# Optimization experiments

Measured on AMD Instinct MI355X. Metric: run time of the kernel, lower is better.

The kernel has to match this reference:

```python
import jax, jax.numpy as jnp
import numpy as np

SCALING = 32.0 / 16.0  # alpha / rank

def setup_inputs() -> dict:
    key = jax.random.key(0)
    ks = jax.random.split(key, 6)
    B, S, D_IN, D_OUT, R, N_ADAPT = 32, 1024, 1024, 4096, 16, 8
    hidden_states = jax.random.normal(ks[0], (B, S, D_IN), dtype=jnp.float32)
    adapter_ids = jax.random.randint(ks[1], (B,), 0, N_ADAPT, dtype=jnp.int32)
    W = jax.random.normal(ks[2], (D_IN, D_OUT), dtype=jnp.float32) * 0.02
    bias = jax.random.normal(ks[3], (D_OUT,), dtype=jnp.float32) * 0.02
    lora_a = jax.random.normal(ks[4], (N_ADAPT, D_IN, R), dtype=jnp.float32) * (1.0 / np.sqrt(D_IN))
    lora_b = jax.random.normal(ks[5], (N_ADAPT, R, D_OUT), dtype=jnp.float32) * 0.02
    return {"hidden_states": hidden_states, "adapter_ids": adapter_ids,
            "W": W, "bias": bias, "lora_a": lora_a, "lora_b": lora_b}

def reference(hidden_states, adapter_ids, W, bias, lora_a, lora_b):
    # Base GPT-2 Conv1D: x @ W + b, W: [in, out]
    base_out = jnp.einsum('bsd,do->bso', hidden_states, W) + bias
    # Per-sample routed LoRA: gather each sample's adapter A/B, then batched low-rank matmuls.
    # Equivalent to the torch loop over unique adapter ids with mask/scatter (dropout=0, eval).
    a_sel = lora_a[adapter_ids]  # [B, d_in, r]
    b_sel = lora_b[adapter_ids]  # [B, r, d_out]
    low_rank = jnp.einsum('bsd,bdr->bsr', hidden_states, a_sel)
    delta = jnp.einsum('bsr,bro->bso', low_rank, b_sel) * SCALING
    return base_out + delta
```

## Files before the change

kernel.cpp:

```cpp
#include <hip/hip_runtime.h>
#include <hip/hip_bf16.h>
#include <stdint.h>

constexpr int kB = 32;
constexpr int kS = 1024;
constexpr int kDin = 1024;
constexpr int kDout = 4096;
constexpr int kRank = 16;
constexpr int kNAdapt = 8;
constexpr int kM = kB * kS;
constexpr float kScale = 2.0f;

typedef __attribute__((ext_vector_type(4))) float f32x4;
typedef __attribute__((ext_vector_type(8))) short s16x8;
typedef __attribute__((ext_vector_type(8))) unsigned short u16x8;
typedef __attribute__((ext_vector_type(4))) unsigned short u16x4;

__device__ __forceinline__ unsigned short f2bf(float f) {
  union { float f; uint32_t u; } x; x.f = f;
  uint32_t u = x.u;
  u += 0x7fffu + ((u >> 16) & 1u);
  return (unsigned short)(u >> 16);
}

__global__ void cast_h_kernel(const float* __restrict__ h, unsigned short* __restrict__ out) {
  size_t i = (size_t)blockIdx.x * blockDim.x + threadIdx.x;
  const f32x4* src = reinterpret_cast<const f32x4*>(h) + i * 2;
  f32x4 v0 = src[0], v1 = src[1];
  u16x8 r;
  r[0] = f2bf(v0[0]); r[1] = f2bf(v0[1]); r[2] = f2bf(v0[2]); r[3] = f2bf(v0[3]);
  r[4] = f2bf(v1[0]); r[5] = f2bf(v1[1]); r[6] = f2bf(v1[2]); r[7] = f2bf(v1[3]);
  *reinterpret_cast<u16x8*>(out + i * 8) = r;
}

__global__ __launch_bounds__(256) void build_weff_kernel(
    const float* __restrict__ W,
    const float* __restrict__ la,
    const float* __restrict__ lb,
    unsigned short* __restrict__ weff) {
  __shared__ float Wt[64][68];
  __shared__ float At[64][20];
  __shared__ float Bt[16][68];
  int bid = blockIdx.x;
  int e = bid & 7;
  int rem = bid >> 3;
  int dt = rem >> 6;
  int ot = rem & 63;
  int d0 = dt * 64, o0 = ot * 64;
  int t = threadIdx.x;
  {
    int r = t >> 4;
    int c = (t & 15) * 4;
    const float* wp = W + (size_t)(d0 + r) * kDout + o0 + c;
#pragma unroll
    for (int p = 0; p < 4; ++p) {
      f32x4 v = *reinterpret_cast<const f32x4*>(wp + (size_t)p * 16 * kDout);
      *reinterpret_cast<f32x4*>(&Wt[p * 16 + r][c]) = v;
    }
  }
  {
    int d = t >> 2, r4 = (t & 3) * 4;
    f32x4 v = *reinterpret_cast<const f32x4*>(la + ((size_t)e * kDin + d0 + d) * kRank + r4);
    *reinterpret_cast<f32x4*>(&At[d][r4]) = v;
  }
  {
    int r = t >> 4, c = (t & 15) * 4;
    f32x4 v = *reinterpret_cast<const f32x4*>(lb + ((size_t)e * kRank + r) * kDout + o0 + c);
    *reinterpret_cast<f32x4*>(&Bt[r][c]) = v;
  }
  __syncthreads();
  int ol_base = t >> 4;
  int dl = (t & 15) * 4;
  f32x4 areg[4][4];
#pragma unroll
  for (int j = 0; j < 4; ++j)
#pragma unroll
    for (int q = 0; q < 4; ++q)
      areg[j][q] = *reinterpret_cast<const f32x4*>(&At[dl + j][q * 4]);
#pragma unroll
  for (int p = 0; p < 4; ++p) {
    int ol = p * 16 + ol_base;
    float bv[kRank];
#pragma unroll
    for (int r = 0; r < kRank; ++r) bv[r] = Bt[r][ol];
    u16x4 r4;
#pragma unroll
    for (int j = 0; j < 4; ++j) {
      float acc = 0.f;
#pragma unroll
      for (int q = 0; q < 4; ++q)
        acc += areg[j][q][0] * bv[q * 4 + 0] + areg[j][q][1] * bv[q * 4 + 1] +
               areg[j][q][2] * bv[q * 4 + 2] + areg[j][q][3] * bv[q * 4 + 3];
      r4[j] = f2bf(Wt[dl + j][ol] + kScale * acc);
    }
    *reinterpret_cast<u16x4*>(weff + ((size_t)e * kDout + o0 + ol) * kDin + d0 + dl) = r4;
  }
}

constexpr int BM = 256, BN = 256, BK = 64;
constexpr int MT2 = kM / BM;
constexpr int NT2 = kDout / BN;
constexpr int NWG2 = MT2 * NT2;

__device__ __forceinline__ void gload16(const unsigned short* g, unsigned short* l) {
  __builtin_amdgcn_global_load_lds((const __attribute__((address_space(1))) void*)g,
                                   (__attribute__((address_space(3))) void*)l, 16, 0, 0);
}

#define STG_A3(sa, h, kk) do { \
  gload16(gA + (size_t)((h) * 128) * kDin + (kk) * 64, ldst + (sa) * 16384 + (h) * 8192); \
  gload16(gA + (size_t)((h) * 128 + 64) * kDin + (kk) * 64, ldst + (sa) * 16384 + (h) * 8192 + 4096); \
} while (0)
#define STG_B3(sb, h, kk) do { \
  gload16(gB + (size_t)((h) * 128) * kDin + (kk) * 64, ldst + 32768 + (sb) * 16384 + (h) * 8192); \
  gload16(gB + (size_t)((h) * 128 + 64) * kDin + (kk) * 64, ldst + 32768 + (sb) * 16384 + (h) * 8192 + 4096); \
} while (0)

#define RD_A(mh, sa) do { _Pragma("unroll") for (int ii = 0; ii < 4; ++ii) { \
  a[ii][0] = *(const s16x8*)&lds[(sa) * 16384 + aRow + ((mh) * 4 + ii) * 1024 + e0]; \
  a[ii][1] = *(const s16x8*)&lds[(sa) * 16384 + aRow + ((mh) * 4 + ii) * 1024 + e1]; } } while (0)
#define RD_B(nh, breg, sb) do { _Pragma("unroll") for (int jj = 0; jj < 2; ++jj) { \
  breg[jj][0] = *(const s16x8*)&lds[32768 + (sb) * 16384 + bRow + ((nh) * 2 + jj) * 1024 + e0]; \
  breg[jj][1] = *(const s16x8*)&lds[32768 + (sb) * 16384 + bRow + ((nh) * 2 + jj) * 1024 + e1]; } } while (0)

#define MM(mh, nh, breg) do { \
  __builtin_amdgcn_s_setprio(1); \
  _Pragma("unroll") for (int ii = 0; ii < 4; ++ii) \
  _Pragma("unroll") for (int jj = 0; jj < 2; ++jj) { \
    acc[(mh) * 4 + ii][(nh) * 2 + jj] = __builtin_amdgcn_mfma_f32_16x16x32_bf16( \
        a[ii][0], breg[jj][0], acc[(mh) * 4 + ii][(nh) * 2 + jj], 0, 0, 0); \
    acc[(mh) * 4 + ii][(nh) * 2 + jj] = __builtin_amdgcn_mfma_f32_16x16x32_bf16( \
        a[ii][1], breg[jj][1], acc[(mh) * 4 + ii][(nh) * 2 + jj], 0, 0, 0); } \
  __builtin_amdgcn_s_setprio(0); \
} while (0)

#define BAR1() do { __builtin_amdgcn_sched_barrier(0); __builtin_amdgcn_s_barrier(); \
  asm volatile("s_waitcnt lgkmcnt(0)" ::: "memory"); __builtin_amdgcn_sched_barrier(0); } while (0)
#define BAR2() do { __builtin_amdgcn_sched_barrier(0); __builtin_amdgcn_s_barrier(); } while (0)
#define VMC(n) asm volatile("s_waitcnt vmcnt(" #n ")" ::: "memory")

__global__ __launch_bounds__(512, 2) void gemm256_kernel(
    const unsigned short* __restrict__ Ab,
    const unsigned short* __restrict__ Weff,
    const float* __restrict__ bias,
    const int* __restrict__ aids,
    float* __restrict__ out) {
  __shared__ unsigned short lds[81920];
  int bid = blockIdx.x;
  int swz = (bid & 7) * (NWG2 / 8) + (bid >> 3);
  int mt = swz >> 4, nt = swz & 15;
  int aid = aids[mt >> 2];
  const unsigned short* Aptr = Ab + (size_t)mt * BM * kDin;
  const unsigned short* Bptr = Weff + ((size_t)aid * kDout + (size_t)nt * BN) * kDin;

  int t = threadIdx.x;
  int l = t & 63;
  int w = t >> 6;
  int wm = w >> 2;
  int wn = w & 3;

  int srcColEl = ((t & 7) * 8) ^ (((t >> 3) & 7) << 3);
  const unsigned short* gA = Aptr + (size_t)(t >> 3) * kDin + srcColEl;
  const unsigned short* gB = Bptr + (size_t)(t >> 3) * kDin + srcColEl;
  unsigned short* ldst = lds + t * 8;

  int xmEl = (l & 7) << 3;
  int e0 = (((l >> 4) * 8) ^ xmEl);
  int e1 = e0 ^ 32;
  int aRow = (wm * 128 + (l & 15)) * 64;
  int bRow = (wn * 64 + (l & 15)) * 64;

  f32x4 acc[8][4];
#pragma unroll
  for (int m = 0; m < 8; ++m)
#pragma unroll
    for (int n = 0; n < 4; ++n) acc[m][n] = f32x4{0.f, 0.f, 0.f, 0.f};
  s16x8 a[4][2], b0[2][2], b1[2][2];

  STG_B3(0, 0, 0); STG_B3(0, 1, 0); STG_A3(0, 0, 0); STG_A3(0, 1, 0);
  STG_B3(1, 0, 1); STG_B3(1, 1, 1); STG_A3(1, 0, 1);
  VMC(6);
  BAR2();

#pragma unroll
  for (int i = 0; i < 8; ++i) {
    const int kt0 = 2 * i, kt1 = 2 * i + 1;
    const int sb0 = kt0 % 3, sb1 = kt1 % 3;
    const int sb2 = (kt0 + 2) % 3, sb3 = (kt1 + 2) % 3;
    const bool last = (i == 7);
    RD_A(0, 0); RD_B(0, b0, sb0);
    if (!last) STG_B3(sb2, 0, kt0 + 2);
    BAR1(); MM(0, 0, b0); BAR2();
    RD_B(1, b1, sb0);
    STG_A3(1, 1, kt1);
    BAR1(); MM(0, 1, b1); BAR2();
    RD_A(1, 0);
    if (!last) STG_B3(sb2, 1, kt0 + 2);
    BAR1(); MM(1, 0, b0); BAR2();
    if (!last) { STG_A3(0, 0, kt0 + 2); VMC(4); } else { VMC(0); }
    BAR1(); MM(1, 1, b1); BAR2();
    RD_A(0, 1); RD_B(0, b0, sb1);
    if (!last) STG_B3(sb3, 0, kt1 + 2);
    BAR1(); MM(0, 0, b0); BAR2();
    RD_B(1, b1, sb1);
    if (!last) STG_A3(0, 1, kt0 + 2);
    BAR1(); MM(0, 1, b1); BAR2();
    RD_A(1, 1);
    if (!last) STG_B3(sb3, 1, kt1 + 2);
    BAR1(); MM(1, 0, b0); BAR2();
    if (!last) { STG_A3(1, 0, kt1 + 2); VMC(4); }
    BAR1(); MM(1, 1, b1); BAR2();
  }

  size_t row0 = (size_t)mt * BM + wm * 128 + (l >> 4) * 4;
  int col0 = nt * BN + wn * 64 + (l & 15);
#pragma unroll
  for (int nf = 0; nf < 4; ++nf) {
    float bv = bias[col0 + nf * 16];
#pragma unroll
    for (int mf = 0; mf < 8; ++mf) {
#pragma unroll
      for (int j = 0; j < 4; ++j)
        out[(row0 + mf * 16 + j) * kDout + col0 + nf * 16] = acc[mf][nf][j] + bv;
    }
  }
}

extern "C" void kernel_launch(void* const* d_in, const int* in_sizes, int n_in,
                              void* d_out, int out_size, void* d_ws, size_t ws_size,
                              hipStream_t stream) {
  const float* h    = (const float*)d_in[0];
  const int*   aids = (const int*)d_in[1];
  const float* W    = (const float*)d_in[2];
  const float* bias = (const float*)d_in[3];
  const float* la   = (const float*)d_in[4];
  const float* lb   = (const float*)d_in[5];
  float* out = (float*)d_out;

  unsigned short* Abf  = (unsigned short*)d_ws;
  unsigned short* Weff = Abf + (size_t)kM * kDin;

  cast_h_kernel<<<(kM * (size_t)kDin / 8) / 256, 256, 0, stream>>>(h, Abf);
  build_weff_kernel<<<kNAdapt * (kDin / 64) * (kDout / 64), 256, 0, stream>>>(W, la, lb, Weff);
  gemm256_kernel<<<NWG2, 512, 0, stream>>>(Abf, Weff, bias, aids, out);
}
```

Measured before the change: 459.5 us.

## Coarsen GEMM pipeline phases: four barrier phases per k-pair with whole-tile staging

Restructures the main GEMM loop from eight barrier-separated MFMA phases per pair of k-tiles to four. Each phase now issues 32 MFMAs covering both B halves. Global-to-LDS staging is regrouped so that each phase issues a full 4-load A or B tile stage rather than half-tile stages. The aim is to cut barrier and waitcnt overhead and give the scheduler longer MFMA runs. In exchange, more LDS reads must complete before each MFMA burst, and prefetch overlap is coarser.

Result: no change. 450.9 us (-1.9%).

```diff
diff --git a/kernel.cpp b/kernel.cpp
--- a/kernel.cpp
+++ b/kernel.cpp
@@ -107,13 +107,17 @@
                                    (__attribute__((address_space(3))) void*)l, 16, 0, 0);
 }
 
-#define STG_A3(sa, h, kk) do { \
-  gload16(gA + (size_t)((h) * 128) * kDin + (kk) * 64, ldst + (sa) * 16384 + (h) * 8192); \
-  gload16(gA + (size_t)((h) * 128 + 64) * kDin + (kk) * 64, ldst + (sa) * 16384 + (h) * 8192 + 4096); \
-} while (0)
-#define STG_B3(sb, h, kk) do { \
-  gload16(gB + (size_t)((h) * 128) * kDin + (kk) * 64, ldst + 32768 + (sb) * 16384 + (h) * 8192); \
-  gload16(gB + (size_t)((h) * 128 + 64) * kDin + (kk) * 64, ldst + 32768 + (sb) * 16384 + (h) * 8192 + 4096); \
+#define STG_A3(sa, kk) do { \
+  gload16(gA + (size_t)0 * kDin + (kk) * 64, ldst + (sa) * 16384); \
+  gload16(gA + (size_t)64 * kDin + (kk) * 64, ldst + (sa) * 16384 + 4096); \
+  gload16(gA + (size_t)128 * kDin + (kk) * 64, ldst + (sa) * 16384 + 8192); \
+  gload16(gA + (size_t)192 * kDin + (kk) * 64, ldst + (sa) * 16384 + 12288); \
+} while (0)
+#define STG_B3(sb, kk) do { \
+  gload16(gB + (size_t)0 * kDin + (kk) * 64, ldst + 32768 + (sb) * 16384); \
+  gload16(gB + (size_t)64 * kDin + (kk) * 64, ldst + 32768 + (sb) * 16384 + 4096); \
+  gload16(gB + (size_t)128 * kDin + (kk) * 64, ldst + 32768 + (sb) * 16384 + 8192); \
+  gload16(gB + (size_t)192 * kDin + (kk) * 64, ldst + 32768 + (sb) * 16384 + 12288); \
 } while (0)
 
 #define RD_A(mh, sa) do { _Pragma("unroll") for (int ii = 0; ii < 4; ++ii) { \
@@ -123,14 +127,18 @@
   breg[jj][0] = *(const s16x8*)&lds[32768 + (sb) * 16384 + bRow + ((nh) * 2 + jj) * 1024 + e0]; \
   breg[jj][1] = *(const s16x8*)&lds[32768 + (sb) * 16384 + bRow + ((nh) * 2 + jj) * 1024 + e1]; } } while (0)
 
-#define MM(mh, nh, breg) do { \
-  __builtin_amdgcn_s_setprio(1); \
+#define MMQ(mh, nh, breg) do { \
   _Pragma("unroll") for (int ii = 0; ii < 4; ++ii) \
   _Pragma("unroll") for (int jj = 0; jj < 2; ++jj) { \
     acc[(mh) * 4 + ii][(nh) * 2 + jj] = __builtin_amdgcn_mfma_f32_16x16x32_bf16( \
         a[ii][0], breg[jj][0], acc[(mh) * 4 + ii][(nh) * 2 + jj], 0, 0, 0); \
     acc[(mh) * 4 + ii][(nh) * 2 + jj] = __builtin_amdgcn_mfma_f32_16x16x32_bf16( \
         a[ii][1], breg[jj][1], acc[(mh) * 4 + ii][(nh) * 2 + jj], 0, 0, 0); } \
+} while (0)
+
+#define MM2(mh) do { \
+  __builtin_amdgcn_s_setprio(1); \
+  MMQ(mh, 0, b0); MMQ(mh, 1, b1); \
   __builtin_amdgcn_s_setprio(0); \
 } while (0)
 
@@ -177,9 +185,8 @@
     for (int n = 0; n < 4; ++n) acc[m][n] = f32x4{0.f, 0.f, 0.f, 0.f};
   s16x8 a[4][2], b0[2][2], b1[2][2];
 
-  STG_B3(0, 0, 0); STG_B3(0, 1, 0); STG_A3(0, 0, 0); STG_A3(0, 1, 0);
-  STG_B3(1, 0, 1); STG_B3(1, 1, 1); STG_A3(1, 0, 1);
-  VMC(6);
+  STG_B3(0, 0); STG_A3(0, 0); STG_B3(1, 1);
+  VMC(4);
   BAR2();
 
 #pragma unroll
@@ -188,28 +195,18 @@
     const int sb0 = kt0 % 3, sb1 = kt1 % 3;
     const int sb2 = (kt0 + 2) % 3, sb3 = (kt1 + 2) % 3;
     const bool last = (i == 7);
-    RD_A(0, 0); RD_B(0, b0, sb0);
-    if (!last) STG_B3(sb2, 0, kt0 + 2);
-    BAR1(); MM(0, 0, b0); BAR2();
-    RD_B(1, b1, sb0);
-    STG_A3(1, 1, kt1);
-    BAR1(); MM(0, 1, b1); BAR2();
+    RD_A(0, 0); RD_B(0, b0, sb0); RD_B(1, b1, sb0);
+    STG_A3(1, kt1);
+    BAR1(); MM2(0); BAR2();
     RD_A(1, 0);
-    if (!last) STG_B3(sb2, 1, kt0 + 2);
-    BAR1(); MM(1, 0, b0); BAR2();
-    if (!last) { STG_A3(0, 0, kt0 + 2); VMC(4); } else { VMC(0); }
-    BAR1(); MM(1, 1, b1); BAR2();
-    RD_A(0, 1); RD_B(0, b0, sb1);
-    if (!last) STG_B3(sb3, 0, kt1 + 2);
-    BAR1(); MM(0, 0, b0); BAR2();
-    RD_B(1, b1, sb1);
-    if (!last) STG_A3(0, 1, kt0 + 2);
-    BAR1(); MM(0, 1, b1); BAR2();
+    if (!last) { STG_B3(sb2, kt0 + 2); VMC(4); } else { VMC(0); }
+    BAR1(); MM2(1); BAR2();
+    RD_A(0, 1); RD_B(0, b0, sb1); RD_B(1, b1, sb1);
+    if (!last) STG_A3(0, kt0 + 2);
+    BAR1(); MM2(0); BAR2();
     RD_A(1, 1);
-    if (!last) STG_B3(sb3, 1, kt1 + 2);
-    BAR1(); MM(1, 0, b0); BAR2();
-    if (!last) { STG_A3(1, 0, kt1 + 2); VMC(4); }
-    BAR1(); MM(1, 1, b1); BAR2();
+    if (!last) { STG_B3(sb3, kt1 + 2); VMC(4); }
+    BAR1(); MM2(1); BAR2();
   }
 
   size_t row0 = (size_t)mt * BM + wm * 128 + (l >> 4) * 4;
```
